# Kernel optimization log

Measured on AMD Instinct MI355X. Metric: run time of the kernel, lower is better.

The kernel has to match this reference:

```python
import jax, jax.numpy as jnp
import numpy as np

B, C_IM, N_IN, H, W = 4, 3, 2, 256, 256
NC, MR, NH, NB = 25, 2, 64, 10  # n_class, m_range, num_hidden, num blocks


def _conv(x, w, pad, dil=1):
    return jax.lax.conv_general_dilated(
        x, w, (1, 1), [(pad, pad), (pad, pad)], rhs_dilation=(dil, dil),
        dimension_numbers=('NCHW', 'OIHW', 'NCHW'))


def _bn(x, g, b, m, v):
    # inference-mode BatchNorm2d, eps=1e-5
    inv = g / jnp.sqrt(v + 1e-5)
    return x * inv[:, None, None] + (b - m * inv)[:, None, None]


def setup_inputs() -> dict:
    key = jax.random.key(0)
    ks = iter(jax.random.split(key, 40))
    rn = lambda s, sc=0.05: jax.random.normal(next(ks), s, jnp.float32) * sc
    ru = lambda s: jax.random.uniform(next(ks), s, jnp.float32)
    return {
        'im_input_f': rn((B, C_IM * N_IN, H, W), 1.0),
        'im_input_b': rn((B, C_IM * N_IN, H, W), 1.0),
        'ones': jnp.ones((B, 1, H, W), jnp.float32),
        'm_kernel': ru((1, NC, 2 * MR + 1, 2 * MR + 1)),
        'bn0_g': ru((C_IM * N_IN,)), 'bn0_b': rn((C_IM * N_IN,)),
        'bn0_m': rn((C_IM * N_IN,)), 'bn0_v': ru((C_IM * N_IN,)),
        'conv0_w': rn((NH, C_IM * N_IN, 3, 3)),
        'blk_bn1_g': ru((NB, NH)), 'blk_bn1_b': rn((NB, NH)),
        'blk_bn1_m': rn((NB, NH)), 'blk_bn1_v': ru((NB, NH)),
        'blk_w11': rn((NB, NH, NH, 3, 3)), 'blk_w12': rn((NB, NH, NH, 3, 3)),
        'blk_bn2_g': ru((NB, NH)), 'blk_bn2_b': rn((NB, NH)),
        'blk_bn2_m': rn((NB, NH)), 'blk_bn2_v': ru((NB, NH)),
        'blk_w2': rn((NB, NH, NH, 3, 3)),
        'bnf_g': ru((NH,)), 'bnf_b': rn((NH,)),
        'bnf_m': rn((NH,)), 'bnf_v': ru((NH,)),
        'convf_w': rn((NC, NH, 3, 3)), 'convf_b': rn((NC,)),
    }


def reference(im_input_f, im_input_b, ones, m_kernel,
              bn0_g, bn0_b, bn0_m, bn0_v, conv0_w,
              blk_bn1_g, blk_bn1_b, blk_bn1_m, blk_bn1_v, blk_w11, blk_w12,
              blk_bn2_g, blk_bn2_b, blk_bn2_m, blk_bn2_v, blk_w2,
              bnf_g, bnf_b, bnf_m, bnf_v, convf_w, convf_b):

    def backbone(x):
        x = _conv(_bn(x, bn0_g, bn0_b, bn0_m, bn0_v), conv0_w, 1)

        def block(h, p):
            g1, b1, m1, v1, w11, w12, g2, b2, m2, v2, w2 = p
            out = jax.nn.relu(_bn(h, g1, b1, m1, v1))
            out = _conv(out, w11, 1) + _conv(out, w12, 2, 2)
            out = _conv(jax.nn.relu(_bn(out, g2, b2, m2, v2)), w2, 1)
            return h + out, None

        x, _ = jax.lax.scan(block, x, (blk_bn1_g, blk_bn1_b, blk_bn1_m,
                                       blk_bn1_v, blk_w11, blk_w12,
                                       blk_bn2_g, blk_bn2_b, blk_bn2_m,
                                       blk_bn2_v, blk_w2))
        return _conv(jax.nn.relu(_bn(x, bnf_g, bnf_b, bnf_m, bnf_v)),
                     convf_w, 1) + convf_b[:, None, None]

    motion_f = backbone(im_input_f)
    motion_b = backbone(im_input_b)
    mask_f = jax.nn.softmax(motion_f, axis=1)  # [B, NC, H, W]
    mask_b = jax.nn.softmax(motion_b, axis=1)

    def seg(mask):  # construct_seg, fully batched
        return _conv(ones * mask, m_kernel, MR)  # [B, 1, H, W]

    def pred_im(im_last, mask):  # construct_image: fold (B, im_channel) into batch
        x = (im_last[:, :, None] * mask[:, None]).reshape(B * C_IM, NC, H, W)
        return _conv(x, m_kernel, MR).reshape(B, C_IM, H, W)

    seg_f = seg(mask_f)
    seg_b = seg(mask_b)
    pred_f = pred_im(im_input_f[:, -C_IM:], mask_f)
    pred_b = pred_im(im_input_b[:, -C_IM:], mask_b)
    attn = (seg_f + 1e-5) / (seg_f + seg_b + 2e-5)
    pred = attn * pred_f + (1 - attn) * pred_b
    return (pred, pred_f, mask_f, attn, pred_b, mask_b, 1 - attn)
```

## Files before the change

kernel.cpp:

```cpp
#include <hip/hip_runtime.h>
#include <stdint.h>

typedef unsigned short u16;
typedef float f4 __attribute__((ext_vector_type(4)));
typedef float f16v __attribute__((ext_vector_type(16)));
typedef short s8v __attribute__((ext_vector_type(8)));

static __device__ __forceinline__ float bf2f(u16 u){ return __uint_as_float(((unsigned)u)<<16); }
static __device__ __forceinline__ u16 f2bf(float f){
  unsigned u = __float_as_uint(f);
  unsigned r = u + 0x7fffu + ((u>>16)&1u);
  return (u16)(r>>16);
}

#define WS_H    0ull
#define WS_TH   67108864ull
#define WS_TL   100663296ull
#define WS_WDH  134217728ull
#define WS_WDL  135692288ull
#define WS_W2H  137166848ull
#define WS_W2L  137904128ull
#define WS_W0T  138641408ull
#define WS_WFH  138655232ull
#define WS_WFL  138692096ull
#define WS_PAR  138728960ull

#define S0 0
#define T0 8
#define S1 16
#define T1 656
#define S2 1296
#define T2 1936
#define SF 2576
#define TF 2640
#define MK 2704
#define CB 3332

#define O_PRED   0ull
#define O_PREDF  786432ull
#define O_MASKF  1572864ull
#define O_ATTN   8126464ull
#define O_PREDB  8388608ull
#define O_MASKB  9175040ull
#define O_OMA    15728640ull

__global__ void k_prep(const float* g0,const float* b0,const float* m0,const float* v0,
                       const float* g1,const float* b1,const float* m1,const float* v1,
                       const float* g2,const float* b2,const float* m2,const float* v2,
                       const float* gf,const float* bf_,const float* mf,const float* vf,
                       const float* mk,const float* cb, float* par){
  for (int i = threadIdx.x; i < 640; i += 256){
    if (i < 6){ float s = g0[i]/sqrtf(v0[i]+1e-5f); par[S0+i]=s; par[T0+i]=b0[i]-m0[i]*s; }
    { float s = g1[i]/sqrtf(v1[i]+1e-5f); par[S1+i]=s; par[T1+i]=b1[i]-m1[i]*s; }
    { float s = g2[i]/sqrtf(v2[i]+1e-5f); par[S2+i]=s; par[T2+i]=b2[i]-m2[i]*s; }
    if (i < 64){ float s = gf[i]/sqrtf(vf[i]+1e-5f); par[SF+i]=s; par[TF+i]=bf_[i]-mf[i]*s; }
    if (i < 625) par[MK+i] = mk[i];
    if (i < 25)  par[CB+i] = cb[i];
  }
}

__global__ void k_wx2(const float* w0, float* w0t){
  int e = blockIdx.x*256 + threadIdx.x;
  if (e < 3456){
    int o = e & 63, r = e >> 6;
    int tap = r % 9, c = r / 9;
    w0t[e] = w0[(o*6+c)*9 + tap];
  }
}

__global__ void k_wxm(const float* w11, const float* w12, const float* w2, const float* wf,
                      u16* wdH, u16* wdL, u16* w2H, u16* w2L, u16* wfH, u16* wfL){
  int e = blockIdx.x*256 + threadIdx.x;
  if (e < 737280){
    int j = e & 7, l = (e>>3) & 63, cog = (e>>9) & 1, kc = (e>>10) & 1;
    int idx2 = e >> 11;
    int tf = idx2 % 36, b = idx2 / 36;
    int tap = tf % 18, h = tf / 18;
    int co = cog*32 + (l & 31);
    int ci = h*32 + kc*16 + (l>>5)*8 + j;
    float w = (tap < 9) ? w11[((b*64+co)*64+ci)*9 + tap]
                        : w12[((b*64+co)*64+ci)*9 + (tap-9)];
    u16 hi = f2bf(w);
    wdH[e] = hi; wdL[e] = f2bf(w - bf2f(hi));
  } else if (e < 1105920){
    int e2 = e - 737280;
    int j = e2 & 7, l = (e2>>3) & 63, cog = (e2>>9) & 1, kc = (e2>>10) & 1;
    int idx2 = e2 >> 11;
    int tf = idx2 % 18, b = idx2 / 18;
    int tap = tf % 9, h = tf / 9;
    int co = cog*32 + (l & 31);
    int ci = h*32 + kc*16 + (l>>5)*8 + j;
    float w = w2[((b*64+co)*64+ci)*9 + tap];
    u16 hi = f2bf(w);
    w2H[e2] = hi; w2L[e2] = f2bf(w - bf2f(hi));
  } else if (e < 1124352){
    int e3 = e - 1105920;
    int j = e3 & 7, l = (e3>>3) & 63, kc = (e3>>9) & 1, tf = e3 >> 10;
    int tap = tf % 9, h = tf / 9;
    int co = l & 31;
    int ci = h*32 + kc*16 + (l>>5)*8 + j;
    float w = (co < 25) ? wf[(co*64+ci)*9 + tap] : 0.f;
    u16 hi = f2bf(w);
    wfH[e3] = hi; wfL[e3] = f2bf(w - bf2f(hi));
  }
}

template<int NT,int TAPSET,int OUTMODE,int NCOG,int INMODE>
__global__ __launch_bounds__(256,2) void k_mc(
    const void* __restrict__ in, const u16* __restrict__ inL,
    float* __restrict__ outb, u16* __restrict__ outH, u16* __restrict__ outL,
    const u16* __restrict__ wH, const u16* __restrict__ wL,
    const float* __restrict__ sc_, const float* __restrict__ tc_,
    const float* __restrict__ osc_, const float* __restrict__ otc_,
    const float* __restrict__ cbv, float* __restrict__ dmask){
  __shared__ __align__(16) u16 ldsH[432*32];
  __shared__ __align__(16) u16 ldsL[432*32];
  __shared__ float lsc[64], ltc[64];
  __shared__ float losc[64], lotc[64];
  const int t = threadIdx.x;
  if (INMODE==0 && t < 64){ lsc[t] = sc_[t]; ltc[t] = tc_[t]; }
  if (OUTMODE==3 && t >= 64 && t < 128){ losc[t-64] = osc_[t-64]; lotc[t-64] = otc_[t-64]; }
  const int img = blockIdx.z, ox = blockIdx.x*32, oy = blockIdx.y*8;
  const int lane = t & 63, wv = t >> 6;
  const int xcol = lane & 31, g = lane >> 5;
  f16v acc[NCOG][2];
  #pragma unroll
  for (int cg=0;cg<NCOG;cg++)
    #pragma unroll
    for (int r=0;r<2;r++) acc[cg][r] = (f16v)(0.f);
  const s8v* wH8 = (const s8v*)wH;
  const s8v* wL8 = (const s8v*)wL;

  #pragma unroll 1
  for (int h = 0; h < 2; ++h){
    __syncthreads();
    for (int idx = t; idx < 1728; idx += 256){
      int oct = idx / 432, px = idx % 432;
      int pr = px / 36, pc = px % 36;
      int gy = oy + pr - 2, gx = ox + pc - 2;
      int cb = h*32 + oct*8;
      s8v vh = {0,0,0,0,0,0,0,0}, vl = {0,0,0,0,0,0,0,0};
      if ((unsigned)gy < 256u && (unsigned)gx < 256u){
        size_t base = (((size_t)(img*64 + cb))<<16) + (size_t)(gy*256 + gx);
        if (INMODE==0){
          const float* ip = (const float*)in + base;
          #pragma unroll
          for (int k=0;k<8;k++){
            float v = fmaxf(ip[(size_t)k<<16]*lsc[cb+k] + ltc[cb+k], 0.f);
            u16 hi = f2bf(v);
            vh[k] = (short)hi;
            vl[k] = (short)f2bf(v - bf2f(hi));
          }
        } else {
          const u16* iph = (const u16*)in + base;
          const u16* ipl = inL + base;
          #pragma unroll
          for (int k=0;k<8;k++){
            vh[k] = (short)iph[(size_t)k<<16];
            vl[k] = (short)ipl[(size_t)k<<16];
          }
        }
      }
      int ad = (px*64 + oct*16) ^ ((px&7)<<4);
      *(s8v*)((char*)ldsH + ad) = vh;
      *(s8v*)((char*)ldsL + ad) = vl;
    }
    __syncthreads();

    #pragma unroll
    for (int tap = 0; tap < NT; ++tap){
      int dy, dx;
      if (TAPSET==0){
        if (tap < 9){ dy = tap/3 - 1; dx = tap%3 - 1; }
        else { int dd = tap-9; dy = 2*(dd/3 - 1); dx = 2*(dd%3 - 1); }
      } else { dy = tap/3 - 1; dx = tap%3 - 1; }
      const int tf = h*NT + tap;
      #pragma unroll
      for (int kc = 0; kc < 2; ++kc){
        s8v ah0, al0, ah1, al1;
        {
          size_t o = (size_t)((tf*2 + kc)*NCOG + 0)*64 + lane;
          ah0 = wH8[o]; al0 = wL8[o];
        }
        if (NCOG==2){
          size_t o = (size_t)((tf*2 + kc)*NCOG + 1)*64 + lane;
          ah1 = wH8[o]; al1 = wL8[o];
        }
        #pragma unroll
        for (int r = 0; r < 2; ++r){
          int px = (wv*2 + r + dy + 2)*36 + (xcol + dx + 2);
          int ad = (px*64 + kc*32 + g*16) ^ ((px&7)<<4);
          s8v xh = *(const s8v*)((const char*)ldsH + ad);
          s8v xl = *(const s8v*)((const char*)ldsL + ad);
          acc[0][r] = __builtin_amdgcn_mfma_f32_32x32x16_bf16(ah0, xh, acc[0][r], 0,0,0);
          if (NCOG==2) acc[1][r] = __builtin_amdgcn_mfma_f32_32x32x16_bf16(ah1, xh, acc[1][r], 0,0,0);
          acc[0][r] = __builtin_amdgcn_mfma_f32_32x32x16_bf16(al0, xh, acc[0][r], 0,0,0);
          if (NCOG==2) acc[1][r] = __builtin_amdgcn_mfma_f32_32x32x16_bf16(al1, xh, acc[1][r], 0,0,0);
          acc[0][r] = __builtin_amdgcn_mfma_f32_32x32x16_bf16(ah0, xl, acc[0][r], 0,0,0);
          if (NCOG==2) acc[1][r] = __builtin_amdgcn_mfma_f32_32x32x16_bf16(ah1, xl, acc[1][r], 0,0,0);
        }
      }
    }
  }

  if (OUTMODE==0 || OUTMODE==1){
    #pragma unroll
    for (int r=0;r<2;r++){
      int y = oy + wv*2 + r;
      int x = ox + xcol;
      #pragma unroll
      for (int cg=0;cg<NCOG;cg++){
        #pragma unroll
        for (int j=0;j<16;j++){
          int co = cg*32 + (j&3) + 8*(j>>2) + 4*g;
          size_t o = (((size_t)(img*64 + co))<<16) + (size_t)(y*256 + x);
          if (OUTMODE==0) outb[o] = acc[cg][r][j];
          else            outb[o] += acc[cg][r][j];
        }
      }
    }
  } else if (OUTMODE==3){
    __syncthreads();
    #pragma unroll
    for (int r=0;r<2;r++){
      int y = oy + wv*2 + r;
      int x = ox + xcol;
      #pragma unroll
      for (int cg=0;cg<NCOG;cg++){
        #pragma unroll
        for (int j=0;j<16;j++){
          int co = cg*32 + (j&3) + 8*(j>>2) + 4*g;
          float v = fmaxf(acc[cg][r][j]*losc[co] + lotc[co], 0.f);
          u16 hi = f2bf(v);
          u16 lo = f2bf(v - bf2f(hi));
          size_t o = (((size_t)(img*64 + co))<<16) + (size_t)(y*256 + x);
          outH[o] = hi;
          outL[o] = lo;
        }
      }
    }
  } else {
    #pragma unroll
    for (int r=0;r<2;r++){
      int y = oy + wv*2 + r;
      int x = ox + xcol;
      float lg[16];
      float mx = -3.4e38f;
      #pragma unroll
      for (int j=0;j<16;j++){
        int co = (j&3) + 8*(j>>2) + 4*g;
        float v = acc[0][r][j] + ((co < 25) ? cbv[co] : 0.f);
        lg[j] = v;
        if (co < 25) mx = fmaxf(mx, v);
      }
      mx = fmaxf(mx, __shfl_xor(mx, 32));
      float s = 0.f;
      #pragma unroll
      for (int j=0;j<16;j++){
        int co = (j&3) + 8*(j>>2) + 4*g;
        float e = (co < 25) ? __expf(lg[j]-mx) : 0.f;
        lg[j] = e; s += e;
      }
      s += __shfl_xor(s, 32);
      float inv = 1.f/s;
      #pragma unroll
      for (int j=0;j<16;j++){
        int co = (j&3) + 8*(j>>2) + 4*g;
        if (co < 25)
          dmask[(((size_t)(img*25+co))<<16) + (size_t)(y*256 + x)] = lg[j]*inv;
      }
    }
  }
}

__global__ __launch_bounds__(256) void k_conv0(
    const float* __restrict__ in, float* __restrict__ outb,
    const float* __restrict__ wt, const float* __restrict__ sc_,
    const float* __restrict__ tc_){
  __shared__ float lin[4*12*20];
  __shared__ float lw[4*9*64];
  __shared__ float lsc[8], ltc[8];
  const int t = threadIdx.x;
  const int img = blockIdx.z;
  const int ox = blockIdx.x*16, oy = blockIdx.y*8;
  if (t < 6){ lsc[t] = sc_[t]; ltc[t] = tc_[t]; }
  const int wv = t>>6, lane = t&63;
  const int row = lane>>4, col = lane&15;
  const int co0 = wv*16;
  const int pb0 = (row+2)*20 + col + 2;
  const int pb1 = pb0 + 80;
  f4 a0[4], a1[4];
  #pragma unroll
  for (int q=0;q<4;q++){ a0[q] = f4{0.f,0.f,0.f,0.f}; a1[q] = f4{0.f,0.f,0.f,0.f}; }

  #pragma unroll 1
  for (int c0=0; c0<6; c0+=4){
    const int cc = (6 - c0 < 4) ? (6 - c0) : 4;
    __syncthreads();
    for (int idx=t; idx<cc*240; idx+=256){
      int c = idx/240, rr = (idx/20)%12, xx = idx%20;
      int gy = oy + rr - 2, gx = ox + xx - 2;
      float v = 0.f;
      if ((unsigned)gy < 256u && (unsigned)gx < 256u)
        v = in[(size_t)(img*6 + c0 + c)*65536 + gy*256 + gx]*lsc[c0+c] + ltc[c0+c];
      lin[idx] = v;
    }
    {
      const f4* ws4 = (const f4*)(wt + (size_t)c0*576);
      f4* lw4 = (f4*)lw;
      for (int idx=t; idx<cc*144; idx+=256) lw4[idx] = ws4[idx];
    }
    __syncthreads();
    #pragma unroll 1
    for (int c=0; c<cc; c++){
      const float* lpc = lin + c*240;
      const float* lwc = lw + c*576 + co0;
      #pragma unroll
      for (int tap=0; tap<9; tap++){
        int dy = tap/3 - 1, dx = tap%3 - 1;
        float v0 = lpc[pb0 + dy*20 + dx];
        float v1 = lpc[pb1 + dy*20 + dx];
        const f4* wp = (const f4*)(lwc + tap*64);
        #pragma unroll
        for (int q=0;q<4;q++){
          f4 w = wp[q];
          a0[q] += v0*w;
          a1[q] += v1*w;
        }
      }
    }
  }

  size_t p0 = (size_t)((oy+row)*256 + ox + col);
  size_t base = (size_t)(img*64 + co0)*65536;
  #pragma unroll
  for (int q=0;q<4;q++)
    #pragma unroll
    for (int j=0;j<4;j++){
      outb[base + (size_t)(q*4+j)*65536 + p0]        = a0[q][j];
      outb[base + (size_t)(q*4+j)*65536 + p0 + 1024] = a1[q][j];
    }
}

__global__ __launch_bounds__(256) void k_blend(const float* __restrict__ msk,
    const float* __restrict__ imf, const float* __restrict__ imb,
    const float* __restrict__ ones_in, const float* __restrict__ par,
    float* __restrict__ out){
  int bid = blockIdx.x;
  int swz = (bid & 7)*128 + (bid >> 3);
  int img = swz >> 8, y = swz & 255, x = threadIdx.x;
  int p = y*256 + x;
  int aofs[25]; unsigned vm = 0u;
  #pragma unroll
  for (int tap=0; tap<25; tap++){
    int dy = tap/5-2, dx = tap%5-2, yy = y+dy, xx = x+dx;
    bool okb = ((unsigned)yy < 256u) && ((unsigned)xx < 256u);
    aofs[tap] = okb ? (yy*256+xx) : 0;
    vm |= (okb ? 1u : 0u) << tap;
  }
  float sff[25], sfb[25];
  #pragma unroll
  for (int i=0;i<25;i++){ sff[i]=0.f; sfb[i]=0.f; }
  #pragma unroll 1
  for (int k=0;k<25;k++){
    const float* mF = msk + O_MASKF + ((size_t)(img*25+k)<<16);
    const float* mB = msk + O_MASKB + ((size_t)(img*25+k)<<16);
    #pragma unroll
    for (int tap=0; tap<25; tap++){
      float mkv = par[MK + k*25 + tap];
      float vF = (vm >> tap & 1u) ? mF[aofs[tap]] : 0.f;
      float vB = (vm >> tap & 1u) ? mB[aofs[tap]] : 0.f;
      sff[tap] += mkv*vF;
      sfb[tap] += mkv*vB;
    }
  }
  float segf = 0.f, segb = 0.f;
  float pf[3] = {0.f,0.f,0.f}, pb[3] = {0.f,0.f,0.f};
  size_t ib = ((size_t)(img*6))<<16;
  #pragma unroll
  for (int tap=0; tap<25; tap++){
    if (vm >> tap & 1u){
      float one = ones_in[((size_t)img<<16) + (size_t)aofs[tap]];
      segf += one*sff[tap]; segb += one*sfb[tap];
      #pragma unroll
      for (int c=0;c<3;c++){
        pf[c] += imf[ib + ((size_t)(3+c)<<16) + (size_t)aofs[tap]] * sff[tap];
        pb[c] += imb[ib + ((size_t)(3+c)<<16) + (size_t)aofs[tap]] * sfb[tap];
      }
    }
  }
  float attn = (segf + 1e-5f)/(segf + segb + 2e-5f);
  float na = 1.f - attn;
  #pragma unroll
  for (int c=0;c<3;c++){
    size_t off = (size_t)(img*3+c)*65536 + p;
    out[O_PRED  + off] = attn*pf[c] + na*pb[c];
    out[O_PREDF + off] = pf[c];
    out[O_PREDB + off] = pb[c];
  }
  size_t oa = ((size_t)img<<16) + (size_t)p;
  out[O_ATTN + oa] = attn;
  out[O_OMA  + oa] = na;
}

extern "C" void kernel_launch(void* const* d_in, const int* in_sizes, int n_in,
                              void* d_out, int out_size, void* d_ws, size_t ws_size,
                              hipStream_t stream){
  (void)in_sizes; (void)n_in; (void)out_size; (void)ws_size;
  char* ws = (char*)d_ws;
  float* h   = (float*)(ws + WS_H);
  u16*  tH   = (u16*)(ws + WS_TH);
  u16*  tL   = (u16*)(ws + WS_TL);
  u16*  wdH  = (u16*)(ws + WS_WDH);
  u16*  wdL  = (u16*)(ws + WS_WDL);
  u16*  w2H  = (u16*)(ws + WS_W2H);
  u16*  w2L  = (u16*)(ws + WS_W2L);
  float* w0t = (float*)(ws + WS_W0T);
  u16*  wfH  = (u16*)(ws + WS_WFH);
  u16*  wfL  = (u16*)(ws + WS_WFL);
  float* par = (float*)(ws + WS_PAR);
  float* out = (float*)d_out;

  k_prep<<<1,256,0,stream>>>((const float*)d_in[4],(const float*)d_in[5],(const float*)d_in[6],(const float*)d_in[7],
                             (const float*)d_in[9],(const float*)d_in[10],(const float*)d_in[11],(const float*)d_in[12],
                             (const float*)d_in[15],(const float*)d_in[16],(const float*)d_in[17],(const float*)d_in[18],
                             (const float*)d_in[20],(const float*)d_in[21],(const float*)d_in[22],(const float*)d_in[23],
                             (const float*)d_in[3],(const float*)d_in[25], par);
  k_wx2<<<14,256,0,stream>>>((const float*)d_in[8], w0t);
  k_wxm<<<4392,256,0,stream>>>((const float*)d_in[13],(const float*)d_in[14],(const float*)d_in[19],
                               (const float*)d_in[24],
                               wdH, wdL, w2H, w2L, wfH, wfL);

  dim3 g0(16,32,4);
  dim3 gm(8,32,4);
  for (int dir=0; dir<2; dir++){
    const float* im = (const float*)d_in[dir];
    float* dmask = out + (dir ? O_MASKB : O_MASKF);
    k_conv0<<<g0,256,0,stream>>>(im, h, w0t, par+S0, par+T0);
    for (int b=0;b<10;b++){
      k_mc<18,0,3,2,0><<<gm,256,0,stream>>>(h, nullptr, nullptr, tH, tL,
          wdH + (size_t)b*73728, wdL + (size_t)b*73728,
          par + S1 + b*64, par + T1 + b*64,
          par + S2 + b*64, par + T2 + b*64, nullptr, nullptr);
      k_mc<9,1,1,2,1><<<gm,256,0,stream>>>(tH, tL, h, nullptr, nullptr,
          w2H + (size_t)b*36864, w2L + (size_t)b*36864,
          nullptr, nullptr, nullptr, nullptr, nullptr, nullptr);
    }
    k_mc<9,1,2,1,0><<<gm,256,0,stream>>>(h, nullptr, nullptr, nullptr, nullptr,
        wfH, wfL, par + SF, par + TF, nullptr, nullptr, par + CB, dmask);
  }
  k_blend<<<1024,256,0,stream>>>(out, (const float*)d_in[0], (const float*)d_in[1],
                                 (const float*)d_in[2], par, out);
}
```

Measured before the change: 4.358 ms.

## Enlarge conv tile to 16 rows, split waves by output-channel group

```diff
diff --git a/kernel.cpp b/kernel.cpp
--- a/kernel.cpp
+++ b/kernel.cpp
@@ -72,33 +72,36 @@
                       u16* wdH, u16* wdL, u16* w2H, u16* w2L, u16* wfH, u16* wfL){
   int e = blockIdx.x*256 + threadIdx.x;
   if (e < 737280){
-    int j = e & 7, l = (e>>3) & 63, cog = (e>>9) & 1, kc = (e>>10) & 1;
-    int idx2 = e >> 11;
-    int tf = idx2 % 36, b = idx2 / 36;
-    int tap = tf % 18, h = tf / 18;
+    int j = e & 7, l = (e>>3) & 63;
+    int rest = e >> 9;
+    int cog = rest & 1; rest >>= 1;
+    int tap = rest % 18, rest3 = rest / 18;
+    int q = rest3 & 3, b = rest3 >> 2;
     int co = cog*32 + (l & 31);
-    int ci = h*32 + kc*16 + (l>>5)*8 + j;
+    int ci = q*16 + (l>>5)*8 + j;
     float w = (tap < 9) ? w11[((b*64+co)*64+ci)*9 + tap]
                         : w12[((b*64+co)*64+ci)*9 + (tap-9)];
     u16 hi = f2bf(w);
     wdH[e] = hi; wdL[e] = f2bf(w - bf2f(hi));
   } else if (e < 1105920){
     int e2 = e - 737280;
-    int j = e2 & 7, l = (e2>>3) & 63, cog = (e2>>9) & 1, kc = (e2>>10) & 1;
-    int idx2 = e2 >> 11;
-    int tf = idx2 % 18, b = idx2 / 18;
-    int tap = tf % 9, h = tf / 9;
+    int j = e2 & 7, l = (e2>>3) & 63;
+    int rest = e2 >> 9;
+    int cog = rest & 1; rest >>= 1;
+    int tap = rest % 9, rest3 = rest / 9;
+    int q = rest3 & 3, b = rest3 >> 2;
     int co = cog*32 + (l & 31);
-    int ci = h*32 + kc*16 + (l>>5)*8 + j;
+    int ci = q*16 + (l>>5)*8 + j;
     float w = w2[((b*64+co)*64+ci)*9 + tap];
     u16 hi = f2bf(w);
     w2H[e2] = hi; w2L[e2] = f2bf(w - bf2f(hi));
   } else if (e < 1124352){
     int e3 = e - 1105920;
-    int j = e3 & 7, l = (e3>>3) & 63, kc = (e3>>9) & 1, tf = e3 >> 10;
-    int tap = tf % 9, h = tf / 9;
+    int j = e3 & 7, l = (e3>>3) & 63;
+    int rest = e3 >> 9;
+    int tap = rest % 9, q = rest / 9;
     int co = l & 31;
-    int ci = h*32 + kc*16 + (l>>5)*8 + j;
+    int ci = q*16 + (l>>5)*8 + j;
     float w = (co < 25) ? wf[(co*64+ci)*9 + tap] : 0.f;
     u16 hi = f2bf(w);
     wfH[e3] = hi; wfL[e3] = f2bf(w - bf2f(hi));
@@ -106,39 +109,40 @@
 }
 
 template<int NT,int TAPSET,int OUTMODE,int NCOG,int INMODE>
-__global__ __launch_bounds__(256,2) void k_mc(
+__global__ __launch_bounds__(512,4) void k_mc(
     const void* __restrict__ in, const u16* __restrict__ inL,
     float* __restrict__ outb, u16* __restrict__ outH, u16* __restrict__ outL,
     const u16* __restrict__ wH, const u16* __restrict__ wL,
     const float* __restrict__ sc_, const float* __restrict__ tc_,
     const float* __restrict__ osc_, const float* __restrict__ otc_,
     const float* __restrict__ cbv, float* __restrict__ dmask){
-  __shared__ __align__(16) u16 ldsH[432*32];
-  __shared__ __align__(16) u16 ldsL[432*32];
+  constexpr int RPW = 2*NCOG;
+  __shared__ __align__(16) u16 ldsH[720*16];
+  __shared__ __align__(16) u16 ldsL[720*16];
   __shared__ float lsc[64], ltc[64];
   __shared__ float losc[64], lotc[64];
   const int t = threadIdx.x;
   if (INMODE==0 && t < 64){ lsc[t] = sc_[t]; ltc[t] = tc_[t]; }
   if (OUTMODE==3 && t >= 64 && t < 128){ losc[t-64] = osc_[t-64]; lotc[t-64] = otc_[t-64]; }
-  const int img = blockIdx.z, ox = blockIdx.x*32, oy = blockIdx.y*8;
+  const int img = blockIdx.z, ox = blockIdx.x*32, oy = blockIdx.y*16;
   const int lane = t & 63, wv = t >> 6;
+  const int cog = (NCOG==2) ? (wv & 1) : 0;
+  const int rh  = (NCOG==2) ? (wv >> 1) : wv;
   const int xcol = lane & 31, g = lane >> 5;
-  f16v acc[NCOG][2];
-  #pragma unroll
-  for (int cg=0;cg<NCOG;cg++)
-    #pragma unroll
-    for (int r=0;r<2;r++) acc[cg][r] = (f16v)(0.f);
+  f16v acc[RPW];
+  #pragma unroll
+  for (int r=0;r<RPW;r++) acc[r] = (f16v)(0.f);
   const s8v* wH8 = (const s8v*)wH;
   const s8v* wL8 = (const s8v*)wL;
 
   #pragma unroll 1
-  for (int h = 0; h < 2; ++h){
+  for (int q = 0; q < 4; ++q){
     __syncthreads();
-    for (int idx = t; idx < 1728; idx += 256){
-      int oct = idx / 432, px = idx % 432;
+    for (int idx = t; idx < 1440; idx += 512){
+      int oct = idx & 1, px = idx >> 1;
       int pr = px / 36, pc = px % 36;
       int gy = oy + pr - 2, gx = ox + pc - 2;
-      int cb = h*32 + oct*8;
+      int cb = q*16 + oct*8;
       s8v vh = {0,0,0,0,0,0,0,0}, vl = {0,0,0,0,0,0,0,0};
       if ((unsigned)gy < 256u && (unsigned)gx < 256u){
         size_t base = (((size_t)(img*64 + cb))<<16) + (size_t)(gy*256 + gx);
@@ -161,7 +165,7 @@
           }
         }
       }
-      int ad = (px*64 + oct*16) ^ ((px&7)<<4);
+      int ad = (px*32 + oct*16) ^ ((px&7)<<4);
       *(s8v*)((char*)ldsH + ad) = vh;
       *(s8v*)((char*)ldsL + ad) = vl;
     }
@@ -174,82 +178,63 @@
         if (tap < 9){ dy = tap/3 - 1; dx = tap%3 - 1; }
         else { int dd = tap-9; dy = 2*(dd/3 - 1); dx = 2*(dd%3 - 1); }
       } else { dy = tap/3 - 1; dx = tap%3 - 1; }
-      const int tf = h*NT + tap;
-      #pragma unroll
-      for (int kc = 0; kc < 2; ++kc){
-        s8v ah0, al0, ah1, al1;
-        {
-          size_t o = (size_t)((tf*2 + kc)*NCOG + 0)*64 + lane;
-          ah0 = wH8[o]; al0 = wL8[o];
-        }
-        if (NCOG==2){
-          size_t o = (size_t)((tf*2 + kc)*NCOG + 1)*64 + lane;
-          ah1 = wH8[o]; al1 = wL8[o];
-        }
-        #pragma unroll
-        for (int r = 0; r < 2; ++r){
-          int px = (wv*2 + r + dy + 2)*36 + (xcol + dx + 2);
-          int ad = (px*64 + kc*32 + g*16) ^ ((px&7)<<4);
-          s8v xh = *(const s8v*)((const char*)ldsH + ad);
-          s8v xl = *(const s8v*)((const char*)ldsL + ad);
-          acc[0][r] = __builtin_amdgcn_mfma_f32_32x32x16_bf16(ah0, xh, acc[0][r], 0,0,0);
-          if (NCOG==2) acc[1][r] = __builtin_amdgcn_mfma_f32_32x32x16_bf16(ah1, xh, acc[1][r], 0,0,0);
-          acc[0][r] = __builtin_amdgcn_mfma_f32_32x32x16_bf16(al0, xh, acc[0][r], 0,0,0);
-          if (NCOG==2) acc[1][r] = __builtin_amdgcn_mfma_f32_32x32x16_bf16(al1, xh, acc[1][r], 0,0,0);
-          acc[0][r] = __builtin_amdgcn_mfma_f32_32x32x16_bf16(ah0, xl, acc[0][r], 0,0,0);
-          if (NCOG==2) acc[1][r] = __builtin_amdgcn_mfma_f32_32x32x16_bf16(ah1, xl, acc[1][r], 0,0,0);
-        }
+      size_t o = (size_t)((q*NT + tap)*NCOG + cog)*64 + lane;
+      s8v ah = wH8[o];
+      s8v al = wL8[o];
+      #pragma unroll
+      for (int r = 0; r < RPW; ++r){
+        int px = (rh*RPW + r + dy + 2)*36 + (xcol + dx + 2);
+        int ad = (px*32 + g*16) ^ ((px&7)<<4);
+        s8v xh = *(const s8v*)((const char*)ldsH + ad);
+        s8v xl = *(const s8v*)((const char*)ldsL + ad);
+        acc[r] = __builtin_amdgcn_mfma_f32_32x32x16_bf16(ah, xh, acc[r], 0,0,0);
+        acc[r] = __builtin_amdgcn_mfma_f32_32x32x16_bf16(al, xh, acc[r], 0,0,0);
+        acc[r] = __builtin_amdgcn_mfma_f32_32x32x16_bf16(ah, xl, acc[r], 0,0,0);
       }
     }
   }
 
   if (OUTMODE==0 || OUTMODE==1){
     #pragma unroll
-    for (int r=0;r<2;r++){
-      int y = oy + wv*2 + r;
+    for (int r=0;r<RPW;r++){
+      int y = oy + rh*RPW + r;
       int x = ox + xcol;
       #pragma unroll
-      for (int cg=0;cg<NCOG;cg++){
-        #pragma unroll
-        for (int j=0;j<16;j++){
-          int co = cg*32 + (j&3) + 8*(j>>2) + 4*g;
-          size_t o = (((size_t)(img*64 + co))<<16) + (size_t)(y*256 + x);
-          if (OUTMODE==0) outb[o] = acc[cg][r][j];
-          else            outb[o] += acc[cg][r][j];
-        }
+      for (int j=0;j<16;j++){
+        int co = cog*32 + (j&3) + 8*(j>>2) + 4*g;
+        size_t o = (((size_t)(img*64 + co))<<16) + (size_t)(y*256 + x);
+        if (OUTMODE==0) outb[o] = acc[r][j];
+        else            outb[o] += acc[r][j];
       }
     }
   } else if (OUTMODE==3){
     __syncthreads();
     #pragma unroll
-    for (int r=0;r<2;r++){
-      int y = oy + wv*2 + r;
+    for (int r=0;r<RPW;r++){
+      int y = oy + rh*RPW + r;
       int x = ox + xcol;
       #pragma unroll
-      for (int cg=0;cg<NCOG;cg++){
-        #pragma unroll
-        for (int j=0;j<16;j++){
-          int co = cg*32 + (j&3) + 8*(j>>2) + 4*g;
-          float v = fmaxf(acc[cg][r][j]*losc[co] + lotc[co], 0.f);
-          u16 hi = f2bf(v);
-          u16 lo = f2bf(v - bf2f(hi));
-          size_t o = (((size_t)(img*64 + co))<<16) + (size_t)(y*256 + x);
-          outH[o] = hi;
-          outL[o] = lo;
-        }
+      for (int j=0;j<16;j++){
+        int co = cog*32 + (j&3) + 8*(j>>2) + 4*g;
+        float v = fmaxf(acc[r][j]*losc[co] + lotc[co], 0.f);
+        u16 hi = f2bf(v);
+        u16 lo = f2bf(v - bf2f(hi));
+        size_t o = (((size_t)(img*64 + co))<<16) + (size_t)(y*256 + x);
+        outH[o] = hi;
+        outL[o] = lo;
       }
     }
   } else {
     #pragma unroll
-    for (int r=0;r<2;r++){
-      int y = oy + wv*2 + r;
+    for (int r=0;r<RPW;r++){
+      int y = oy + rh*RPW + r;
       int x = ox + xcol;
       float lg[16];
       float mx = -3.4e38f;
       #pragma unroll
       for (int j=0;j<16;j++){
         int co = (j&3) + 8*(j>>2) + 4*g;
-        float v = acc[0][r][j] + ((co < 25) ? cbv[co] : 0.f);
+        float v = acc[r][j] + ((co < 25) ? cbv[co] : 0.f);
         lg[j] = v;
         if (co < 25) mx = fmaxf(mx, v);
       }
@@ -432,21 +417,21 @@
                                wdH, wdL, w2H, w2L, wfH, wfL);
 
   dim3 g0(16,32,4);
-  dim3 gm(8,32,4);
+  dim3 gm(8,16,4);
   for (int dir=0; dir<2; dir++){
     const float* im = (const float*)d_in[dir];
     float* dmask = out + (dir ? O_MASKB : O_MASKF);
     k_conv0<<<g0,256,0,stream>>>(im, h, w0t, par+S0, par+T0);
     for (int b=0;b<10;b++){
-      k_mc<18,0,3,2,0><<<gm,256,0,stream>>>(h, nullptr, nullptr, tH, tL,
+      k_mc<18,0,3,2,0><<<gm,512,0,stream>>>(h, nullptr, nullptr, tH, tL,
           wdH + (size_t)b*73728, wdL + (size_t)b*73728,
           par + S1 + b*64, par + T1 + b*64,
           par + S2 + b*64, par + T2 + b*64, nullptr, nullptr);
-      k_mc<9,1,1,2,1><<<gm,256,0,stream>>>(tH, tL, h, nullptr, nullptr,
+      k_mc<9,1,1,2,1><<<gm,512,0,stream>>>(tH, tL, h, nullptr, nullptr,
           w2H + (size_t)b*36864, w2L + (size_t)b*36864,
           nullptr, nullptr, nullptr, nullptr, nullptr, nullptr);
     }
-    k_mc<9,1,2,1,0><<<gm,256,0,stream>>>(h, nullptr, nullptr, nullptr, nullptr,
+    k_mc<9,1,2,1,0><<<gm,512,0,stream>>>(h, nullptr, nullptr, nullptr, nullptr,
         wfH, wfL, par + SF, par + TF, nullptr, nullptr, par + CB, dmask);
   }
   k_blend<<<1024,256,0,stream>>>(out, (const float*)d_in[0], (const float*)d_in[1],
```

New measurement: 9.243 ms. 2.12x slower.

## Stage input channels in 16-channel chunks to halve LDS and raise occupancy

Applied to the files above, without the earlier changes.

```diff
diff --git a/kernel.cpp b/kernel.cpp
--- a/kernel.cpp
+++ b/kernel.cpp
@@ -72,33 +72,36 @@
                       u16* wdH, u16* wdL, u16* w2H, u16* w2L, u16* wfH, u16* wfL){
   int e = blockIdx.x*256 + threadIdx.x;
   if (e < 737280){
-    int j = e & 7, l = (e>>3) & 63, cog = (e>>9) & 1, kc = (e>>10) & 1;
-    int idx2 = e >> 11;
-    int tf = idx2 % 36, b = idx2 / 36;
-    int tap = tf % 18, h = tf / 18;
+    int j = e & 7, l = (e>>3) & 63;
+    int rest = e >> 9;
+    int cog = rest & 1; rest >>= 1;
+    int tap = rest % 18, rest3 = rest / 18;
+    int q = rest3 & 3, b = rest3 >> 2;
     int co = cog*32 + (l & 31);
-    int ci = h*32 + kc*16 + (l>>5)*8 + j;
+    int ci = q*16 + (l>>5)*8 + j;
     float w = (tap < 9) ? w11[((b*64+co)*64+ci)*9 + tap]
                         : w12[((b*64+co)*64+ci)*9 + (tap-9)];
     u16 hi = f2bf(w);
     wdH[e] = hi; wdL[e] = f2bf(w - bf2f(hi));
   } else if (e < 1105920){
     int e2 = e - 737280;
-    int j = e2 & 7, l = (e2>>3) & 63, cog = (e2>>9) & 1, kc = (e2>>10) & 1;
-    int idx2 = e2 >> 11;
-    int tf = idx2 % 18, b = idx2 / 18;
-    int tap = tf % 9, h = tf / 9;
+    int j = e2 & 7, l = (e2>>3) & 63;
+    int rest = e2 >> 9;
+    int cog = rest & 1; rest >>= 1;
+    int tap = rest % 9, rest3 = rest / 9;
+    int q = rest3 & 3, b = rest3 >> 2;
     int co = cog*32 + (l & 31);
-    int ci = h*32 + kc*16 + (l>>5)*8 + j;
+    int ci = q*16 + (l>>5)*8 + j;
     float w = w2[((b*64+co)*64+ci)*9 + tap];
     u16 hi = f2bf(w);
     w2H[e2] = hi; w2L[e2] = f2bf(w - bf2f(hi));
   } else if (e < 1124352){
     int e3 = e - 1105920;
-    int j = e3 & 7, l = (e3>>3) & 63, kc = (e3>>9) & 1, tf = e3 >> 10;
-    int tap = tf % 9, h = tf / 9;
+    int j = e3 & 7, l = (e3>>3) & 63;
+    int rest = e3 >> 9;
+    int tap = rest % 9, q = rest / 9;
     int co = l & 31;
-    int ci = h*32 + kc*16 + (l>>5)*8 + j;
+    int ci = q*16 + (l>>5)*8 + j;
     float w = (co < 25) ? wf[(co*64+ci)*9 + tap] : 0.f;
     u16 hi = f2bf(w);
     wfH[e3] = hi; wfL[e3] = f2bf(w - bf2f(hi));
@@ -106,15 +109,15 @@
 }
 
 template<int NT,int TAPSET,int OUTMODE,int NCOG,int INMODE>
-__global__ __launch_bounds__(256,2) void k_mc(
+__global__ __launch_bounds__(256,4) void k_mc(
     const void* __restrict__ in, const u16* __restrict__ inL,
     float* __restrict__ outb, u16* __restrict__ outH, u16* __restrict__ outL,
     const u16* __restrict__ wH, const u16* __restrict__ wL,
     const float* __restrict__ sc_, const float* __restrict__ tc_,
     const float* __restrict__ osc_, const float* __restrict__ otc_,
     const float* __restrict__ cbv, float* __restrict__ dmask){
-  __shared__ __align__(16) u16 ldsH[432*32];
-  __shared__ __align__(16) u16 ldsL[432*32];
+  __shared__ __align__(16) u16 ldsH[432*16];
+  __shared__ __align__(16) u16 ldsL[432*16];
   __shared__ float lsc[64], ltc[64];
   __shared__ float losc[64], lotc[64];
   const int t = threadIdx.x;
@@ -132,13 +135,13 @@
   const s8v* wL8 = (const s8v*)wL;
 
   #pragma unroll 1
-  for (int h = 0; h < 2; ++h){
+  for (int q = 0; q < 4; ++q){
     __syncthreads();
-    for (int idx = t; idx < 1728; idx += 256){
-      int oct = idx / 432, px = idx % 432;
+    for (int idx = t; idx < 864; idx += 256){
+      int oct = idx & 1, px = idx >> 1;
       int pr = px / 36, pc = px % 36;
       int gy = oy + pr - 2, gx = ox + pc - 2;
-      int cb = h*32 + oct*8;
+      int cb = q*16 + oct*8;
       s8v vh = {0,0,0,0,0,0,0,0}, vl = {0,0,0,0,0,0,0,0};
       if ((unsigned)gy < 256u && (unsigned)gx < 256u){
         size_t base = (((size_t)(img*64 + cb))<<16) + (size_t)(gy*256 + gx);
@@ -161,7 +164,7 @@
           }
         }
       }
-      int ad = (px*64 + oct*16) ^ ((px&7)<<4);
+      int ad = (px*32 + oct*16) ^ ((px&7)<<4);
       *(s8v*)((char*)ldsH + ad) = vh;
       *(s8v*)((char*)ldsL + ad) = vl;
     }
@@ -174,31 +177,26 @@
         if (tap < 9){ dy = tap/3 - 1; dx = tap%3 - 1; }
         else { int dd = tap-9; dy = 2*(dd/3 - 1); dx = 2*(dd%3 - 1); }
       } else { dy = tap/3 - 1; dx = tap%3 - 1; }
-      const int tf = h*NT + tap;
-      #pragma unroll
-      for (int kc = 0; kc < 2; ++kc){
-        s8v ah0, al0, ah1, al1;
-        {
-          size_t o = (size_t)((tf*2 + kc)*NCOG + 0)*64 + lane;
-          ah0 = wH8[o]; al0 = wL8[o];
-        }
-        if (NCOG==2){
-          size_t o = (size_t)((tf*2 + kc)*NCOG + 1)*64 + lane;
-          ah1 = wH8[o]; al1 = wL8[o];
-        }
-        #pragma unroll
-        for (int r = 0; r < 2; ++r){
-          int px = (wv*2 + r + dy + 2)*36 + (xcol + dx + 2);
-          int ad = (px*64 + kc*32 + g*16) ^ ((px&7)<<4);
-          s8v xh = *(const s8v*)((const char*)ldsH + ad);
-          s8v xl = *(const s8v*)((const char*)ldsL + ad);
-          acc[0][r] = __builtin_amdgcn_mfma_f32_32x32x16_bf16(ah0, xh, acc[0][r], 0,0,0);
-          if (NCOG==2) acc[1][r] = __builtin_amdgcn_mfma_f32_32x32x16_bf16(ah1, xh, acc[1][r], 0,0,0);
-          acc[0][r] = __builtin_amdgcn_mfma_f32_32x32x16_bf16(al0, xh, acc[0][r], 0,0,0);
-          if (NCOG==2) acc[1][r] = __builtin_amdgcn_mfma_f32_32x32x16_bf16(al1, xh, acc[1][r], 0,0,0);
-          acc[0][r] = __builtin_amdgcn_mfma_f32_32x32x16_bf16(ah0, xl, acc[0][r], 0,0,0);
-          if (NCOG==2) acc[1][r] = __builtin_amdgcn_mfma_f32_32x32x16_bf16(ah1, xl, acc[1][r], 0,0,0);
-        }
+      size_t o0 = (size_t)((q*NT + tap)*NCOG + 0)*64 + lane;
+      s8v ah0 = wH8[o0];
+      s8v al0 = wL8[o0];
+      s8v ah1, al1;
+      if (NCOG==2){
+        ah1 = wH8[o0 + 64];
+        al1 = wL8[o0 + 64];
+      }
+      #pragma unroll
+      for (int r = 0; r < 2; ++r){
+        int px = (wv*2 + r + dy + 2)*36 + (xcol + dx + 2);
+        int ad = (px*32 + g*16) ^ ((px&7)<<4);
+        s8v xh = *(const s8v*)((const char*)ldsH + ad);
+        s8v xl = *(const s8v*)((const char*)ldsL + ad);
+        acc[0][r] = __builtin_amdgcn_mfma_f32_32x32x16_bf16(ah0, xh, acc[0][r], 0,0,0);
+        if (NCOG==2) acc[1][r] = __builtin_amdgcn_mfma_f32_32x32x16_bf16(ah1, xh, acc[1][r], 0,0,0);
+        acc[0][r] = __builtin_amdgcn_mfma_f32_32x32x16_bf16(al0, xh, acc[0][r], 0,0,0);
+        if (NCOG==2) acc[1][r] = __builtin_amdgcn_mfma_f32_32x32x16_bf16(al1, xh, acc[1][r], 0,0,0);
+        acc[0][r] = __builtin_amdgcn_mfma_f32_32x32x16_bf16(ah0, xl, acc[0][r], 0,0,0);
+        if (NCOG==2) acc[1][r] = __builtin_amdgcn_mfma_f32_32x32x16_bf16(ah1, xl, acc[1][r], 0,0,0);
       }
     }
   }
```

Measured after the change: 5.244 ms. 20.3% more time.
